# Kernel tuning notes

Hardware: AMD Instinct MI355X
Metric: run time of the kernel (lower is better)

## Reference

```python
import jax, jax.numpy as jnp
import numpy as np

N_NODES = 30000
IN_DIM = 8
HIDDEN = 64
HEADS1 = 8
OUT_DIM = 8
NEG_SLOPE = 0.2


def _glorot(key, shape):
    fan_in, fan_out = shape[0], shape[-1]
    lim = jnp.sqrt(6.0 / (fan_in + fan_out))
    return jax.random.uniform(key, shape, jnp.float32, -lim, lim)


def setup_inputs() -> dict:
    key = jax.random.key(0)
    ks = jax.random.split(key, 12)
    x = jax.random.normal(ks[0], (N_NODES, IN_DIM), jnp.float32)
    edge_index = jax.random.randint(ks[1], (2, 300000), 0, N_NODES, jnp.int32)
    # layer 1: in=8, out=HIDDEN per head, 8 heads, concat
    W1l = _glorot(ks[2], (IN_DIM, HEADS1 * HIDDEN))
    W1r = _glorot(ks[3], (IN_DIM, HEADS1 * HIDDEN))
    a1 = _glorot(ks[4], (HEADS1, HIDDEN))
    b1 = jnp.zeros((HEADS1 * HIDDEN,), jnp.float32)
    # layer 2: in=HEADS1*HIDDEN, out=OUT_DIM, 1 head
    W2l = _glorot(ks[5], (HEADS1 * HIDDEN, OUT_DIM))
    W2r = _glorot(ks[6], (HEADS1 * HIDDEN, OUT_DIM))
    a2 = _glorot(ks[7], (1, OUT_DIM))
    b2 = jnp.zeros((OUT_DIM,), jnp.float32)
    return {"x": x, "edge_index": edge_index, "W1l": W1l, "W1r": W1r,
            "a1": a1, "b1": b1, "W2l": W2l, "W2r": W2r, "a2": a2, "b2": b2}


def gatv2_layer(x, src, dst, Wl, Wr, att, bias, heads, out_ch):
    n = x.shape[0]
    xl = (x @ Wl).reshape(n, heads, out_ch)   # messages (source side)
    xr = (x @ Wr).reshape(n, heads, out_ch)   # target side
    h = jax.nn.leaky_relu(xl[src] + xr[dst], NEG_SLOPE)   # [E,H,C]
    e = jnp.einsum('ehc,hc->eh', h, att)                  # [E,H]
    # segment softmax over incoming edges per destination node
    m = jax.ops.segment_max(e, dst, num_segments=n)
    p = jnp.exp(e - m[dst])
    denom = jax.ops.segment_sum(p, dst, num_segments=n)
    alpha = p / denom[dst]                                # [E,H]
    out = jax.ops.segment_sum(alpha[..., None] * xl[src], dst, num_segments=n)
    return out.reshape(n, heads * out_ch) + bias


def reference(x, edge_index, W1l, W1r, a1, b1, W2l, W2r, a2, b2):
    n = x.shape[0]
    loops = jnp.arange(n, dtype=edge_index.dtype)
    src = jnp.concatenate([edge_index[0], loops])  # add_self_loops=True (PyG default)
    dst = jnp.concatenate([edge_index[1], loops])
    h = gatv2_layer(x, src, dst, W1l, W1r, a1, b1, HEADS1, HIDDEN)
    h = jax.nn.relu(h)
    out = gatv2_layer(h, src, dst, W2l, W2r, a2, b2, 1, OUT_DIM)
    return out
```

## Files before the change

### kernel.cpp

```cpp
#include <hip/hip_runtime.h>
#include <math.h>

#define N_NODES   30000
#define N_EDGE    300000
#define N_EDGE_T  330000
#define HEADS     8
#define HIDDEN    64
#define IN_DIM    8
#define OUT_DIM   8
#define NEG_SLOPE 0.2f

typedef float v2f __attribute__((ext_vector_type(2)));


__global__ __launch_bounds__(256) void count_kernel(const int* __restrict__ ei,
                                                    int* __restrict__ count) {
    int e = blockIdx.x * 256 + threadIdx.x;
    if (e >= N_EDGE_T) return;
    int d = (e < N_EDGE) ? ei[N_EDGE + e] : (e - N_EDGE);
    atomicAdd(&count[d], 1);
}

__global__ __launch_bounds__(1024) void scan_kernel(const int* __restrict__ count,
                                                    int* __restrict__ row_start,
                                                    int* __restrict__ cursor) {
    __shared__ int wsum[16];
    const int tid  = threadIdx.x;
    const int wave = tid >> 6;
    const int lane = tid & 63;
    const int4* c4 = (const int4*)count;
    const int N4 = N_NODES / 4;
    int run = 0;
    for (int r = 0; r < 4; ++r) {
        const int g  = r * 1024 + tid;
        const int i0 = 2 * g;
        const int i1 = 2 * g + 1;
        int4 v0 = make_int4(0,0,0,0), v1 = make_int4(0,0,0,0);
        if (i0 < N4) v0 = c4[i0];
        if (i1 < N4) v1 = c4[i1];
        int s = v0.x + v0.y + v0.z + v0.w + v1.x + v1.y + v1.z + v1.w;
        int sc = s;
        #pragma unroll
        for (int off = 1; off < 64; off <<= 1) {
            int t = __shfl_up(sc, off, 64);
            if (lane >= off) sc += t;
        }
        if (lane == 63) wsum[wave] = sc;
        __syncthreads();
        if (tid < 16) {
            int w = wsum[tid];
            #pragma unroll
            for (int off = 1; off < 16; off <<= 1) {
                int t = __shfl_up(w, off, 64);
                if (tid >= off) w += t;
            }
            wsum[tid] = w;
        }
        __syncthreads();
        const int woff = (wave > 0) ? wsum[wave - 1] : 0;
        int e0 = run + woff + (sc - s);
        int4 ex0, ex1;
        ex0.x = e0;           ex0.y = ex0.x + v0.x;
        ex0.z = ex0.y + v0.y; ex0.w = ex0.z + v0.z;
        int e4 = ex0.w + v0.w;
        ex1.x = e4;           ex1.y = ex1.x + v1.x;
        ex1.z = ex1.y + v1.y; ex1.w = ex1.z + v1.z;
        if (i0 < N4) { ((int4*)row_start)[i0] = ex0; ((int4*)cursor)[i0] = ex0; }
        if (i1 < N4) { ((int4*)row_start)[i1] = ex1; ((int4*)cursor)[i1] = ex1; }
        const int tot = wsum[15];
        __syncthreads();
        run += tot;
    }
    if (tid == 0) row_start[N_NODES] = run;
}

__global__ __launch_bounds__(256) void scatter_kernel(const int* __restrict__ ei,
                                                      int* __restrict__ cursor,
                                                      int* __restrict__ edge_src) {
    int e = blockIdx.x * 256 + threadIdx.x;
    if (e >= N_EDGE_T) return;
    int s, d;
    if (e < N_EDGE) { s = ei[e]; d = ei[N_EDGE + e]; }
    else            { s = d = e - N_EDGE; }
    int pos = atomicAdd(&cursor[d], 1);
    edge_src[pos] = s;
}


__global__ __launch_bounds__(128, 4) void layer1_kernel(
    const float* __restrict__ x,
    const float* __restrict__ W1l, const float* __restrict__ W1r,
    const float* __restrict__ a1,  const float* __restrict__ b1,
    const float* __restrict__ W2l, const float* __restrict__ W2r,
    const int* __restrict__ row_start, const int* __restrict__ edge_src,
    float* __restrict__ xl2, float* __restrict__ xr2)
{
    const int d    = blockIdx.x;
    const int tid  = threadIdx.x;
    const int head = tid >> 4;
    const int c4   = tid & 15;
    const int colb = head * HIDDEN + c4 * 4;

    v2f wl[IN_DIM][2], av[2];
    #pragma unroll
    for (int k = 0; k < IN_DIM; ++k) {
        const float4 l4 = *(const float4*)&W1l[k * 512 + colb];
        wl[k][0] = v2f{l4.x, l4.y};
        wl[k][1] = v2f{l4.z, l4.w};
    }
    { const float4 a4 = *(const float4*)&a1[colb];
      av[0] = v2f{a4.x, a4.y}; av[1] = v2f{a4.z, a4.w}; }

    v2f xr[2] = {v2f{0.f, 0.f}, v2f{0.f, 0.f}};
    #pragma unroll
    for (int k = 0; k < IN_DIM; ++k) {
        const float xv = x[d * IN_DIM + k];
        const float4 r4 = *(const float4*)&W1r[k * 512 + colb];
        v2f xs = {xv, xv};
        xr[0] = __builtin_elementwise_fma(xs, v2f{r4.x, r4.y}, xr[0]);
        xr[1] = __builtin_elementwise_fma(xs, v2f{r4.z, r4.w}, xr[1]);
    }

    const int rs = row_start[d];
    const int re = row_start[d + 1];

    float denom = 0.f;
    v2f acc[2] = {v2f{0.f, 0.f}, v2f{0.f, 0.f}};

    float xc[4][IN_DIM];
    #pragma unroll
    for (int i = 0; i < 4; ++i) {
        int idx = rs + i; if (idx > re - 1) idx = re - 1;
        int si = __builtin_amdgcn_readfirstlane(edge_src[idx]);
        #pragma unroll
        for (int k = 0; k < IN_DIM; ++k) xc[i][k] = x[si * IN_DIM + k];
    }

    for (int base = rs;; base += 4) {
        const int  nb   = base + 4;
        const bool more = nb < re;
        float xn[4][IN_DIM];
        if (more) {
            #pragma unroll
            for (int i = 0; i < 4; ++i) {
                int idx = nb + i; if (idx > re - 1) idx = re - 1;
                int si = __builtin_amdgcn_readfirstlane(edge_src[idx]);
                #pragma unroll
                for (int k = 0; k < IN_DIM; ++k) xn[i][k] = x[si * IN_DIM + k];
            }
        }

        v2f xl[4][2];
        #pragma unroll
        for (int e = 0; e < 4; ++e) { xl[e][0] = v2f{0.f, 0.f}; xl[e][1] = v2f{0.f, 0.f}; }
        #pragma unroll
        for (int k = 0; k < IN_DIM; ++k) {
            #pragma unroll
            for (int e = 0; e < 4; ++e) {
                v2f xs = {xc[e][k], xc[e][k]};
                xl[e][0] = __builtin_elementwise_fma(xs, wl[k][0], xl[e][0]);
                xl[e][1] = __builtin_elementwise_fma(xs, wl[k][1], xl[e][1]);
            }
        }

        float eh[4];
        #pragma unroll
        for (int e = 0; e < 4; ++e) {
            v2f v0 = xl[e][0] + xr[0];
            v2f v1 = xl[e][1] + xr[1];
            v2f t0 = __builtin_elementwise_max(v0, v0 * NEG_SLOPE);
            v2f t1 = __builtin_elementwise_max(v1, v1 * NEG_SLOPE);
            v2f s2 = __builtin_elementwise_fma(av[1], t1, av[0] * t0);
            eh[e] = s2.x + s2.y;
        }
        #pragma unroll
        for (int off = 1; off < 16; off <<= 1) {
            #pragma unroll
            for (int e = 0; e < 4; ++e) eh[e] += __shfl_xor(eh[e], off, 64);
        }

        float p[4];
        #pragma unroll
        for (int e = 0; e < 4; ++e)
            p[e] = (base + e < re) ? __expf(eh[e]) : 0.f;

        denom += (p[0] + p[1]) + (p[2] + p[3]);
        #pragma unroll
        for (int j = 0; j < 2; ++j) {
            v2f a = acc[j];
            #pragma unroll
            for (int e = 0; e < 4; ++e) {
                v2f ps = {p[e], p[e]};
                a = __builtin_elementwise_fma(ps, xl[e][j], a);
            }
            acc[j] = a;
        }

        if (!more) break;
        #pragma unroll
        for (int i = 0; i < 4; ++i) {
            #pragma unroll
            for (int k = 0; k < IN_DIM; ++k) xc[i][k] = xn[i][k];
        }
    }

    const float inv = 1.f / denom;
    const float4 b4 = *(const float4*)&b1[colb];
    float hv[4];
    hv[0] = fmaxf(acc[0].x * inv + b4.x, 0.f);
    hv[1] = fmaxf(acc[0].y * inv + b4.y, 0.f);
    hv[2] = fmaxf(acc[1].x * inv + b4.z, 0.f);
    hv[3] = fmaxf(acc[1].y * inv + b4.w, 0.f);

    float vl[OUT_DIM], vr[OUT_DIM];
    #pragma unroll
    for (int j = 0; j < OUT_DIM; ++j) { vl[j] = 0.f; vr[j] = 0.f; }
    #pragma unroll
    for (int i = 0; i < 4; ++i) {
        const float4 l0 = *(const float4*)&W2l[(colb + i) * OUT_DIM];
        const float4 l1 = *(const float4*)&W2l[(colb + i) * OUT_DIM + 4];
        const float4 r0 = *(const float4*)&W2r[(colb + i) * OUT_DIM];
        const float4 r1 = *(const float4*)&W2r[(colb + i) * OUT_DIM + 4];
        vl[0] = fmaf(hv[i], l0.x, vl[0]); vl[1] = fmaf(hv[i], l0.y, vl[1]);
        vl[2] = fmaf(hv[i], l0.z, vl[2]); vl[3] = fmaf(hv[i], l0.w, vl[3]);
        vl[4] = fmaf(hv[i], l1.x, vl[4]); vl[5] = fmaf(hv[i], l1.y, vl[5]);
        vl[6] = fmaf(hv[i], l1.z, vl[6]); vl[7] = fmaf(hv[i], l1.w, vl[7]);
        vr[0] = fmaf(hv[i], r0.x, vr[0]); vr[1] = fmaf(hv[i], r0.y, vr[1]);
        vr[2] = fmaf(hv[i], r0.z, vr[2]); vr[3] = fmaf(hv[i], r0.w, vr[3]);
        vr[4] = fmaf(hv[i], r1.x, vr[4]); vr[5] = fmaf(hv[i], r1.y, vr[5]);
        vr[6] = fmaf(hv[i], r1.z, vr[6]); vr[7] = fmaf(hv[i], r1.w, vr[7]);
    }
    #pragma unroll
    for (int off = 1; off < 16; off <<= 1) {
        #pragma unroll
        for (int j = 0; j < OUT_DIM; ++j) {
            vl[j] += __shfl_xor(vl[j], off, 64);
            vr[j] += __shfl_xor(vr[j], off, 64);
        }
    }

    __shared__ float psl[HEADS][OUT_DIM];
    __shared__ float psr[HEADS][OUT_DIM];
    if (c4 == 0) {
        #pragma unroll
        for (int j = 0; j < OUT_DIM; ++j) { psl[head][j] = vl[j]; psr[head][j] = vr[j]; }
    }
    __syncthreads();
    if (tid < 16) {
        const int side = tid >> 3, j = tid & 7;
        float s = 0.f;
        if (side == 0) {
            #pragma unroll
            for (int h = 0; h < HEADS; ++h) s += psl[h][j];
            xl2[d * OUT_DIM + j] = s;
        } else {
            #pragma unroll
            for (int h = 0; h < HEADS; ++h) s += psr[h][j];
            xr2[d * OUT_DIM + j] = s;
        }
    }
}


__global__ __launch_bounds__(256) void layer2_kernel(
    const float* __restrict__ xl2, const float* __restrict__ xr2,
    const float* __restrict__ a2,  const float* __restrict__ b2,
    const int* __restrict__ row_start, const int* __restrict__ edge_src,
    float* __restrict__ out)
{
    const int wave = threadIdx.x >> 6;
    const int lane = threadIdx.x & 63;
    const int d = blockIdx.x * 4 + wave;
    if (d >= N_NODES) return;
    const int sub = lane >> 3;
    const int c   = lane & 7;

    const float a_c  = a2[c];
    const float xr_d = xr2[d * OUT_DIM + c];

    const int rs = row_start[d];
    const int re = row_start[d + 1];

    float denom = 0.f, acc = 0.f;

    for (int base = rs; base < re; base += 8) {
        int e = base + sub;
        bool valid = (e < re);
        int s = valid ? edge_src[e] : 0;
        float xls = xl2[s * OUT_DIM + c];
        float v = xls + xr_d;
        float t = fmaxf(v, NEG_SLOPE * v);
        float eh = a_c * t;
        eh += __shfl_xor(eh, 1, 64);
        eh += __shfl_xor(eh, 2, 64);
        eh += __shfl_xor(eh, 4, 64);
        float p = valid ? __expf(eh) : 0.f;
        denom += p;
        acc = fmaf(p, xls, acc);
    }

    denom += __shfl_xor(denom, 8,  64);  acc += __shfl_xor(acc, 8,  64);
    denom += __shfl_xor(denom, 16, 64);  acc += __shfl_xor(acc, 16, 64);
    denom += __shfl_xor(denom, 32, 64);  acc += __shfl_xor(acc, 32, 64);

    if (sub == 0) out[d * OUT_DIM + c] = acc / denom + b2[c];
}


extern "C" void kernel_launch(void* const* d_in, const int* in_sizes, int n_in,
                              void* d_out, int out_size, void* d_ws, size_t ws_size,
                              hipStream_t stream) {
    const float* x   = (const float*)d_in[0];
    const int*   ei  = (const int*)  d_in[1];
    const float* W1l = (const float*)d_in[2];
    const float* W1r = (const float*)d_in[3];
    const float* a1  = (const float*)d_in[4];
    const float* b1  = (const float*)d_in[5];
    const float* W2l = (const float*)d_in[6];
    const float* W2r = (const float*)d_in[7];
    const float* a2  = (const float*)d_in[8];
    const float* b2  = (const float*)d_in[9];
    float* out = (float*)d_out;

    char* ws = (char*)d_ws;
    size_t off = 0;
    auto carve = [&](size_t bytes) { char* p = ws + off; off += (bytes + 255) & ~size_t(255); return p; };
    int*   count     = (int*)  carve(N_NODES * sizeof(int));
    int*   row_start = (int*)  carve((N_NODES + 1) * sizeof(int));
    int*   cursor    = (int*)  carve(N_NODES * sizeof(int));
    int*   edge_src  = (int*)  carve((N_EDGE_T + 8) * sizeof(int));
    float* xl2       = (float*)carve(N_NODES * OUT_DIM * sizeof(float));
    float* xr2       = (float*)carve(N_NODES * OUT_DIM * sizeof(float));

    hipMemsetAsync(count, 0, N_NODES * sizeof(int), stream);
    count_kernel  <<<(N_EDGE_T + 255) / 256, 256, 0, stream>>>(ei, count);
    scan_kernel   <<<1, 1024, 0, stream>>>(count, row_start, cursor);
    scatter_kernel<<<(N_EDGE_T + 255) / 256, 256, 0, stream>>>(ei, cursor, edge_src);
    layer1_kernel <<<N_NODES, 128, 0, stream>>>(x, W1l, W1r, a1, b1, W2l, W2r,
                                                row_start, edge_src, xl2, xr2);
    layer2_kernel <<<(N_NODES + 3) / 4, 256, 0, stream>>>(xl2, xr2, a2, b2,
                                                          row_start, edge_src, out);
}
```

Measured before the change: 269.1 us.

## Pre-gather source features into CSR edge order during scatter

The scatter kernel now copies each edge's 8-float source feature vector into an edge-ordered buffer alongside the CSR index. Layer 1 then streams those features contiguously instead of doing a dependent edge_src load followed by an indirect x load. This removes a serialized latency chain from the hot aggregation loop. In exchange it adds roughly 10 MB of extra writes in the scatter kernel and a larger workspace. The loop also now reads up to three entries past each row's end, relying on masked weights and the buffer padding.

```diff
diff --git a/kernel.cpp b/kernel.cpp
--- a/kernel.cpp
+++ b/kernel.cpp
@@ -76,7 +76,9 @@
 
 __global__ __launch_bounds__(256) void scatter_kernel(const int* __restrict__ ei,
                                                       int* __restrict__ cursor,
-                                                      int* __restrict__ edge_src) {
+                                                      int* __restrict__ edge_src,
+                                                      const float* __restrict__ x,
+                                                      float* __restrict__ xg) {
     int e = blockIdx.x * 256 + threadIdx.x;
     if (e >= N_EDGE_T) return;
     int s, d;
@@ -84,6 +86,10 @@
     else            { s = d = e - N_EDGE; }
     int pos = atomicAdd(&cursor[d], 1);
     edge_src[pos] = s;
+    const float4* xs = (const float4*)(x + s * IN_DIM);
+    float4 a = xs[0], b = xs[1];
+    float4* dst = (float4*)(xg + pos * IN_DIM);
+    dst[0] = a; dst[1] = b;
 }
 
 
@@ -92,7 +98,7 @@
     const float* __restrict__ W1l, const float* __restrict__ W1r,
     const float* __restrict__ a1,  const float* __restrict__ b1,
     const float* __restrict__ W2l, const float* __restrict__ W2r,
-    const int* __restrict__ row_start, const int* __restrict__ edge_src,
+    const int* __restrict__ row_start, const float* __restrict__ xg,
     float* __restrict__ xl2, float* __restrict__ xr2)
 {
     const int d    = blockIdx.x;
@@ -121,35 +127,36 @@
         xr[1] = __builtin_elementwise_fma(xs, v2f{r4.z, r4.w}, xr[1]);
     }
 
-    const int rs = row_start[d];
-    const int re = row_start[d + 1];
+    const int rs = __builtin_amdgcn_readfirstlane(row_start[d]);
+    const int re = __builtin_amdgcn_readfirstlane(row_start[d + 1]);
 
     float denom = 0.f;
     v2f acc[2] = {v2f{0.f, 0.f}, v2f{0.f, 0.f}};
 
-    float xc[4][IN_DIM];
-    #pragma unroll
-    for (int i = 0; i < 4; ++i) {
-        int idx = rs + i; if (idx > re - 1) idx = re - 1;
-        int si = __builtin_amdgcn_readfirstlane(edge_src[idx]);
-        #pragma unroll
-        for (int k = 0; k < IN_DIM; ++k) xc[i][k] = x[si * IN_DIM + k];
-    }
+    const float4* g = (const float4*)xg;
+
+    float4 xc[4][2];
+    #pragma unroll
+    for (int i = 0; i < 4; ++i) { xc[i][0] = g[(rs + i) * 2]; xc[i][1] = g[(rs + i) * 2 + 1]; }
 
     for (int base = rs;; base += 4) {
-        const int  nb   = base + 4;
-        const bool more = nb < re;
-        float xn[4][IN_DIM];
+        const bool more = base + 4 < re;
+        float4 xn[4][2];
         if (more) {
             #pragma unroll
             for (int i = 0; i < 4; ++i) {
-                int idx = nb + i; if (idx > re - 1) idx = re - 1;
-                int si = __builtin_amdgcn_readfirstlane(edge_src[idx]);
-                #pragma unroll
-                for (int k = 0; k < IN_DIM; ++k) xn[i][k] = x[si * IN_DIM + k];
+                xn[i][0] = g[(base + 4 + i) * 2];
+                xn[i][1] = g[(base + 4 + i) * 2 + 1];
             }
         }
 
+        float xf[4][IN_DIM];
+        #pragma unroll
+        for (int e = 0; e < 4; ++e) {
+            xf[e][0] = xc[e][0].x; xf[e][1] = xc[e][0].y; xf[e][2] = xc[e][0].z; xf[e][3] = xc[e][0].w;
+            xf[e][4] = xc[e][1].x; xf[e][5] = xc[e][1].y; xf[e][6] = xc[e][1].z; xf[e][7] = xc[e][1].w;
+        }
+
         v2f xl[4][2];
         #pragma unroll
         for (int e = 0; e < 4; ++e) { xl[e][0] = v2f{0.f, 0.f}; xl[e][1] = v2f{0.f, 0.f}; }
@@ -157,7 +164,7 @@
         for (int k = 0; k < IN_DIM; ++k) {
             #pragma unroll
             for (int e = 0; e < 4; ++e) {
-                v2f xs = {xc[e][k], xc[e][k]};
+                v2f xs = {xf[e][k], xf[e][k]};
                 xl[e][0] = __builtin_elementwise_fma(xs, wl[k][0], xl[e][0]);
                 xl[e][1] = __builtin_elementwise_fma(xs, wl[k][1], xl[e][1]);
             }
@@ -198,10 +205,7 @@
 
         if (!more) break;
         #pragma unroll
-        for (int i = 0; i < 4; ++i) {
-            #pragma unroll
-            for (int k = 0; k < IN_DIM; ++k) xc[i][k] = xn[i][k];
-        }
+        for (int i = 0; i < 4; ++i) { xc[i][0] = xn[i][0]; xc[i][1] = xn[i][1]; }
     }
 
     const float inv = 1.f / denom;
@@ -329,15 +333,16 @@
     int*   row_start = (int*)  carve((N_NODES + 1) * sizeof(int));
     int*   cursor    = (int*)  carve(N_NODES * sizeof(int));
     int*   edge_src  = (int*)  carve((N_EDGE_T + 8) * sizeof(int));
+    float* xg        = (float*)carve((N_EDGE_T + 8) * IN_DIM * sizeof(float));
     float* xl2       = (float*)carve(N_NODES * OUT_DIM * sizeof(float));
     float* xr2       = (float*)carve(N_NODES * OUT_DIM * sizeof(float));
 
     hipMemsetAsync(count, 0, N_NODES * sizeof(int), stream);
     count_kernel  <<<(N_EDGE_T + 255) / 256, 256, 0, stream>>>(ei, count);
     scan_kernel   <<<1, 1024, 0, stream>>>(count, row_start, cursor);
-    scatter_kernel<<<(N_EDGE_T + 255) / 256, 256, 0, stream>>>(ei, cursor, edge_src);
+    scatter_kernel<<<(N_EDGE_T + 255) / 256, 256, 0, stream>>>(ei, cursor, edge_src, x, xg);
     layer1_kernel <<<N_NODES, 128, 0, stream>>>(x, W1l, W1r, a1, b1, W2l, W2r,
-                                                row_start, edge_src, xl2, xr2);
+                                                row_start, xg, xl2, xr2);
     layer2_kernel <<<(N_NODES + 3) / 4, 256, 0, stream>>>(xl2, xr2, a2, b2,
                                                           row_start, edge_src, out);
 }
```

New measurement: 274.7 us. 1.02x slower.

## Stage neighbor features in LDS, process two nodes per block, transpose-reduce outputs

Applied to the files above, without the earlier changes.

Layer 1 now processes two destination nodes per 256-thread block. Each block cooperatively gathers up to 64 neighbor feature rows into shared memory with one parallel load, replacing the serialized per-edge prefetch chain. Edges beyond 64 fall back to direct global loads. The final 16-value head reduction becomes a recursive-halving shuffle exchange, cutting shuffle count. The cost is an extra block barrier, more LDS use, and a clamped over-fetch for short rows.

```diff
diff --git a/kernel.cpp b/kernel.cpp
--- a/kernel.cpp
+++ b/kernel.cpp
@@ -9,6 +9,7 @@
 #define IN_DIM    8
 #define OUT_DIM   8
 #define NEG_SLOPE 0.2f
+#define MAX_STAGE 64
 
 typedef float v2f __attribute__((ext_vector_type(2)));
 
@@ -87,7 +88,53 @@
 }
 
 
-__global__ __launch_bounds__(128, 4) void layer1_kernel(
+__device__ __forceinline__ void l1_batch(const float xf[4][IN_DIM],
+                                         const v2f wl[IN_DIM][2],
+                                         const v2f av0, const v2f av1,
+                                         const v2f xr0, const v2f xr1,
+                                         int nvalid,
+                                         float& denom, v2f& acc0, v2f& acc1)
+{
+    v2f xl[4][2];
+    #pragma unroll
+    for (int e = 0; e < 4; ++e) { xl[e][0] = v2f{0.f, 0.f}; xl[e][1] = v2f{0.f, 0.f}; }
+    #pragma unroll
+    for (int k = 0; k < IN_DIM; ++k) {
+        #pragma unroll
+        for (int e = 0; e < 4; ++e) {
+            v2f xs = {xf[e][k], xf[e][k]};
+            xl[e][0] = __builtin_elementwise_fma(xs, wl[k][0], xl[e][0]);
+            xl[e][1] = __builtin_elementwise_fma(xs, wl[k][1], xl[e][1]);
+        }
+    }
+    float eh[4];
+    #pragma unroll
+    for (int e = 0; e < 4; ++e) {
+        v2f v0 = xl[e][0] + xr0;
+        v2f v1 = xl[e][1] + xr1;
+        v2f t0 = __builtin_elementwise_max(v0, v0 * NEG_SLOPE);
+        v2f t1 = __builtin_elementwise_max(v1, v1 * NEG_SLOPE);
+        v2f s2 = __builtin_elementwise_fma(av1, t1, av0 * t0);
+        eh[e] = s2.x + s2.y;
+    }
+    #pragma unroll
+    for (int off = 1; off < 16; off <<= 1) {
+        #pragma unroll
+        for (int e = 0; e < 4; ++e) eh[e] += __shfl_xor(eh[e], off, 64);
+    }
+    float p[4];
+    #pragma unroll
+    for (int e = 0; e < 4; ++e) p[e] = (e < nvalid) ? __expf(eh[e]) : 0.f;
+    denom += (p[0] + p[1]) + (p[2] + p[3]);
+    #pragma unroll
+    for (int e = 0; e < 4; ++e) {
+        v2f ps = {p[e], p[e]};
+        acc0 = __builtin_elementwise_fma(ps, xl[e][0], acc0);
+        acc1 = __builtin_elementwise_fma(ps, xl[e][1], acc1);
+    }
+}
+
+__global__ __launch_bounds__(256, 4) void layer1_kernel(
     const float* __restrict__ x,
     const float* __restrict__ W1l, const float* __restrict__ W1r,
     const float* __restrict__ a1,  const float* __restrict__ b1,
@@ -95,13 +142,30 @@
     const int* __restrict__ row_start, const int* __restrict__ edge_src,
     float* __restrict__ xl2, float* __restrict__ xr2)
 {
-    const int d    = blockIdx.x;
+    __shared__ float lds_x[2][MAX_STAGE][IN_DIM];
+    __shared__ float lds_red[2][HEADS][16];
+
     const int tid  = threadIdx.x;
-    const int head = tid >> 4;
-    const int c4   = tid & 15;
+    const int node = tid >> 7;
+    const int t128 = tid & 127;
+    const int head = t128 >> 4;
+    const int c4   = t128 & 15;
+    const int d    = blockIdx.x * 2 + node;
     const int colb = head * HIDDEN + c4 * 4;
 
-    v2f wl[IN_DIM][2], av[2];
+    const int rs = row_start[d];
+    const int re = row_start[d + 1];
+    const int rowlen = re - rs;
+
+    {
+        const int slot = t128 >> 1, half = t128 & 1;
+        int idx = rs + slot; if (idx > N_EDGE_T - 1) idx = N_EDGE_T - 1;
+        const int s = edge_src[idx];
+        const float4 v = *(const float4*)(x + s * IN_DIM + half * 4);
+        *(float4*)&lds_x[node][slot][half * 4] = v;
+    }
+
+    v2f wl[IN_DIM][2], av0, av1;
     #pragma unroll
     for (int k = 0; k < IN_DIM; ++k) {
         const float4 l4 = *(const float4*)&W1l[k * 512 + colb];
@@ -109,155 +173,118 @@
         wl[k][1] = v2f{l4.z, l4.w};
     }
     { const float4 a4 = *(const float4*)&a1[colb];
-      av[0] = v2f{a4.x, a4.y}; av[1] = v2f{a4.z, a4.w}; }
-
-    v2f xr[2] = {v2f{0.f, 0.f}, v2f{0.f, 0.f}};
+      av0 = v2f{a4.x, a4.y}; av1 = v2f{a4.z, a4.w}; }
+
+    v2f xr0 = v2f{0.f, 0.f}, xr1 = v2f{0.f, 0.f};
     #pragma unroll
     for (int k = 0; k < IN_DIM; ++k) {
         const float xv = x[d * IN_DIM + k];
         const float4 r4 = *(const float4*)&W1r[k * 512 + colb];
         v2f xs = {xv, xv};
-        xr[0] = __builtin_elementwise_fma(xs, v2f{r4.x, r4.y}, xr[0]);
-        xr[1] = __builtin_elementwise_fma(xs, v2f{r4.z, r4.w}, xr[1]);
-    }
-
-    const int rs = row_start[d];
-    const int re = row_start[d + 1];
+        xr0 = __builtin_elementwise_fma(xs, v2f{r4.x, r4.y}, xr0);
+        xr1 = __builtin_elementwise_fma(xs, v2f{r4.z, r4.w}, xr1);
+    }
+
+    __syncthreads();
 
     float denom = 0.f;
-    v2f acc[2] = {v2f{0.f, 0.f}, v2f{0.f, 0.f}};
-
-    float xc[4][IN_DIM];
-    #pragma unroll
-    for (int i = 0; i < 4; ++i) {
-        int idx = rs + i; if (idx > re - 1) idx = re - 1;
-        int si = __builtin_amdgcn_readfirstlane(edge_src[idx]);
-        #pragma unroll
-        for (int k = 0; k < IN_DIM; ++k) xc[i][k] = x[si * IN_DIM + k];
-    }
-
-    for (int base = rs;; base += 4) {
-        const int  nb   = base + 4;
-        const bool more = nb < re;
-        float xn[4][IN_DIM];
-        if (more) {
-            #pragma unroll
-            for (int i = 0; i < 4; ++i) {
-                int idx = nb + i; if (idx > re - 1) idx = re - 1;
-                int si = __builtin_amdgcn_readfirstlane(edge_src[idx]);
-                #pragma unroll
-                for (int k = 0; k < IN_DIM; ++k) xn[i][k] = x[si * IN_DIM + k];
-            }
-        }
-
-        v2f xl[4][2];
-        #pragma unroll
-        for (int e = 0; e < 4; ++e) { xl[e][0] = v2f{0.f, 0.f}; xl[e][1] = v2f{0.f, 0.f}; }
-        #pragma unroll
-        for (int k = 0; k < IN_DIM; ++k) {
-            #pragma unroll
-            for (int e = 0; e < 4; ++e) {
-                v2f xs = {xc[e][k], xc[e][k]};
-                xl[e][0] = __builtin_elementwise_fma(xs, wl[k][0], xl[e][0]);
-                xl[e][1] = __builtin_elementwise_fma(xs, wl[k][1], xl[e][1]);
-            }
-        }
-
-        float eh[4];
+    v2f acc0 = v2f{0.f, 0.f}, acc1 = v2f{0.f, 0.f};
+
+    const int n_stage = rowlen < MAX_STAGE ? rowlen : MAX_STAGE;
+    for (int base = 0; base < n_stage; base += 4) {
+        float xf[4][IN_DIM];
         #pragma unroll
         for (int e = 0; e < 4; ++e) {
-            v2f v0 = xl[e][0] + xr[0];
-            v2f v1 = xl[e][1] + xr[1];
-            v2f t0 = __builtin_elementwise_max(v0, v0 * NEG_SLOPE);
-            v2f t1 = __builtin_elementwise_max(v1, v1 * NEG_SLOPE);
-            v2f s2 = __builtin_elementwise_fma(av[1], t1, av[0] * t0);
-            eh[e] = s2.x + s2.y;
-        }
-        #pragma unroll
-        for (int off = 1; off < 16; off <<= 1) {
-            #pragma unroll
-            for (int e = 0; e < 4; ++e) eh[e] += __shfl_xor(eh[e], off, 64);
-        }
-
-        float p[4];
-        #pragma unroll
-        for (int e = 0; e < 4; ++e)
-            p[e] = (base + e < re) ? __expf(eh[e]) : 0.f;
-
-        denom += (p[0] + p[1]) + (p[2] + p[3]);
-        #pragma unroll
-        for (int j = 0; j < 2; ++j) {
-            v2f a = acc[j];
-            #pragma unroll
-            for (int e = 0; e < 4; ++e) {
-                v2f ps = {p[e], p[e]};
-                a = __builtin_elementwise_fma(ps, xl[e][j], a);
-            }
-            acc[j] = a;
-        }
-
-        if (!more) break;
-        #pragma unroll
-        for (int i = 0; i < 4; ++i) {
-            #pragma unroll
-            for (int k = 0; k < IN_DIM; ++k) xc[i][k] = xn[i][k];
-        }
+            int slot = base + e; if (slot > MAX_STAGE - 1) slot = MAX_STAGE - 1;
+            const float4 u0 = *(const float4*)&lds_x[node][slot][0];
+            const float4 u1 = *(const float4*)&lds_x[node][slot][4];
+            xf[e][0] = u0.x; xf[e][1] = u0.y; xf[e][2] = u0.z; xf[e][3] = u0.w;
+            xf[e][4] = u1.x; xf[e][5] = u1.y; xf[e][6] = u1.z; xf[e][7] = u1.w;
+        }
+        l1_batch(xf, wl, av0, av1, xr0, xr1, rowlen - base, denom, acc0, acc1);
+    }
+    for (int base = MAX_STAGE; base < rowlen; base += 4) {
+        float xf[4][IN_DIM];
+        #pragma unroll
+        for (int e = 0; e < 4; ++e) {
+            int idx = rs + base + e; if (idx > re - 1) idx = re - 1;
+            const int s = edge_src[idx];
+            const float4 u0 = *(const float4*)(x + s * IN_DIM);
+            const float4 u1 = *(const float4*)(x + s * IN_DIM + 4);
+            xf[e][0] = u0.x; xf[e][1] = u0.y; xf[e][2] = u0.z; xf[e][3] = u0.w;
+            xf[e][4] = u1.x; xf[e][5] = u1.y; xf[e][6] = u1.z; xf[e][7] = u1.w;
+        }
+        l1_batch(xf, wl, av0, av1, xr0, xr1, rowlen - base, denom, acc0, acc1);
     }
 
     const float inv = 1.f / denom;
     const float4 b4 = *(const float4*)&b1[colb];
     float hv[4];
-    hv[0] = fmaxf(acc[0].x * inv + b4.x, 0.f);
-    hv[1] = fmaxf(acc[0].y * inv + b4.y, 0.f);
-    hv[2] = fmaxf(acc[1].x * inv + b4.z, 0.f);
-    hv[3] = fmaxf(acc[1].y * inv + b4.w, 0.f);
-
-    float vl[OUT_DIM], vr[OUT_DIM];
-    #pragma unroll
-    for (int j = 0; j < OUT_DIM; ++j) { vl[j] = 0.f; vr[j] = 0.f; }
+    hv[0] = fmaxf(acc0.x * inv + b4.x, 0.f);
+    hv[1] = fmaxf(acc0.y * inv + b4.y, 0.f);
+    hv[2] = fmaxf(acc1.x * inv + b4.z, 0.f);
+    hv[3] = fmaxf(acc1.y * inv + b4.w, 0.f);
+
+    float w[16];
+    #pragma unroll
+    for (int j = 0; j < 16; ++j) w[j] = 0.f;
     #pragma unroll
     for (int i = 0; i < 4; ++i) {
         const float4 l0 = *(const float4*)&W2l[(colb + i) * OUT_DIM];
         const float4 l1 = *(const float4*)&W2l[(colb + i) * OUT_DIM + 4];
         const float4 r0 = *(const float4*)&W2r[(colb + i) * OUT_DIM];
         const float4 r1 = *(const float4*)&W2r[(colb + i) * OUT_DIM + 4];
-        vl[0] = fmaf(hv[i], l0.x, vl[0]); vl[1] = fmaf(hv[i], l0.y, vl[1]);
-        vl[2] = fmaf(hv[i], l0.z, vl[2]); vl[3] = fmaf(hv[i], l0.w, vl[3]);
-        vl[4] = fmaf(hv[i], l1.x, vl[4]); vl[5] = fmaf(hv[i], l1.y, vl[5]);
-        vl[6] = fmaf(hv[i], l1.z, vl[6]); vl[7] = fmaf(hv[i], l1.w, vl[7]);
-        vr[0] = fmaf(hv[i], r0.x, vr[0]); vr[1] = fmaf(hv[i], r0.y, vr[1]);
-        vr[2] = fmaf(hv[i], r0.z, vr[2]); vr[3] = fmaf(hv[i], r0.w, vr[3]);
-        vr[4] = fmaf(hv[i], r1.x, vr[4]); vr[5] = fmaf(hv[i], r1.y, vr[5]);
-        vr[6] = fmaf(hv[i], r1.z, vr[6]); vr[7] = fmaf(hv[i], r1.w, vr[7]);
-    }
-    #pragma unroll
-    for (int off = 1; off < 16; off <<= 1) {
-        #pragma unroll
-        for (int j = 0; j < OUT_DIM; ++j) {
-            vl[j] += __shfl_xor(vl[j], off, 64);
-            vr[j] += __shfl_xor(vr[j], off, 64);
-        }
-    }
-
-    __shared__ float psl[HEADS][OUT_DIM];
-    __shared__ float psr[HEADS][OUT_DIM];
-    if (c4 == 0) {
-        #pragma unroll
-        for (int j = 0; j < OUT_DIM; ++j) { psl[head][j] = vl[j]; psr[head][j] = vr[j]; }
-    }
+        w[0]  = fmaf(hv[i], l0.x, w[0]);  w[1]  = fmaf(hv[i], l0.y, w[1]);
+        w[2]  = fmaf(hv[i], l0.z, w[2]);  w[3]  = fmaf(hv[i], l0.w, w[3]);
+        w[4]  = fmaf(hv[i], l1.x, w[4]);  w[5]  = fmaf(hv[i], l1.y, w[5]);
+        w[6]  = fmaf(hv[i], l1.z, w[6]);  w[7]  = fmaf(hv[i], l1.w, w[7]);
+        w[8]  = fmaf(hv[i], r0.x, w[8]);  w[9]  = fmaf(hv[i], r0.y, w[9]);
+        w[10] = fmaf(hv[i], r0.z, w[10]); w[11] = fmaf(hv[i], r0.w, w[11]);
+        w[12] = fmaf(hv[i], r1.x, w[12]); w[13] = fmaf(hv[i], r1.y, w[13]);
+        w[14] = fmaf(hv[i], r1.z, w[14]); w[15] = fmaf(hv[i], r1.w, w[15]);
+    }
+    {
+        const bool up = (c4 & 8) != 0;
+        #pragma unroll
+        for (int i = 0; i < 8; ++i) {
+            float send = up ? w[i] : w[i + 8];
+            float recv = __shfl_xor(send, 8, 64);
+            w[i] = (up ? w[i + 8] : w[i]) + recv;
+        }
+    }
+    {
+        const bool up = (c4 & 4) != 0;
+        #pragma unroll
+        for (int i = 0; i < 4; ++i) {
+            float send = up ? w[i] : w[i + 4];
+            float recv = __shfl_xor(send, 4, 64);
+            w[i] = (up ? w[i + 4] : w[i]) + recv;
+        }
+    }
+    {
+        const bool up = (c4 & 2) != 0;
+        #pragma unroll
+        for (int i = 0; i < 2; ++i) {
+            float send = up ? w[i] : w[i + 2];
+            float recv = __shfl_xor(send, 2, 64);
+            w[i] = (up ? w[i + 2] : w[i]) + recv;
+        }
+    }
+    {
+        const bool up = (c4 & 1) != 0;
+        float send = up ? w[0] : w[1];
+        float recv = __shfl_xor(send, 1, 64);
+        w[0] = (up ? w[1] : w[0]) + recv;
+    }
+    lds_red[node][head][c4] = w[0];
     __syncthreads();
-    if (tid < 16) {
-        const int side = tid >> 3, j = tid & 7;
+    if (t128 < 16) {
         float s = 0.f;
-        if (side == 0) {
-            #pragma unroll
-            for (int h = 0; h < HEADS; ++h) s += psl[h][j];
-            xl2[d * OUT_DIM + j] = s;
-        } else {
-            #pragma unroll
-            for (int h = 0; h < HEADS; ++h) s += psr[h][j];
-            xr2[d * OUT_DIM + j] = s;
-        }
+        #pragma unroll
+        for (int h = 0; h < HEADS; ++h) s += lds_red[node][h][t128];
+        const int side = t128 >> 3, j = t128 & 7;
+        if (side == 0) xl2[d * OUT_DIM + j] = s;
+        else           xr2[d * OUT_DIM + j] = s;
     }
 }
 
@@ -336,8 +363,8 @@
     count_kernel  <<<(N_EDGE_T + 255) / 256, 256, 0, stream>>>(ei, count);
     scan_kernel   <<<1, 1024, 0, stream>>>(count, row_start, cursor);
     scatter_kernel<<<(N_EDGE_T + 255) / 256, 256, 0, stream>>>(ei, cursor, edge_src);
-    layer1_kernel <<<N_NODES, 128, 0, stream>>>(x, W1l, W1r, a1, b1, W2l, W2r,
-                                                row_start, edge_src, xl2, xr2);
+    layer1_kernel <<<N_NODES / 2, 256, 0, stream>>>(x, W1l, W1r, a1, b1, W2l, W2r,
+                                                    row_start, edge_src, xl2, xr2);
     layer2_kernel <<<(N_NODES + 3) / 4, 256, 0, stream>>>(xl2, xr2, a2, b2,
                                                           row_start, edge_src, out);
 }
```

New measurement: 277.5 us. +3.1%, slower.
